# Kernel optimization log

Hardware: AMD Instinct MI355X
Metric: run time of the kernel (lower is better)

The kernel has to match this reference:

```python
import jax, jax.numpy as jnp
import numpy as np

# ---- hyperparameters (from pars / init_kwargs) ----
ALPHA = 0.9          # synaptic conductance decay (snn.Synaptic alpha)
BETA = 0.8           # membrane decay (snn.Synaptic beta)
BETA_PLUS = 0.9      # pre-synaptic trace decay
BETA_MINUS = 0.9     # post-synaptic trace decay
THRESHOLD = 1.0
W_MIN, W_MAX = 0.0, 1.0
A_PLUS, A_MINUS = 0.008, 0.0008
T, B, IN, N = 350, 128, 784, 400
SPIKE_P = 0.05       # Bernoulli firing probability of the rate-coded input


def setup_inputs() -> dict:
    key = jax.random.key(0)
    k_img, k_w = jax.random.split(key)
    # Poisson/Bernoulli rate-coded MNIST spike train [T, B, IN]
    image = (jax.random.uniform(k_img, (T, B, IN)) < SPIKE_P).astype(jnp.float32)
    # nn.Linear default init U(-1/sqrt(IN), 1/sqrt(IN)) then clamp to [w_min, w_max]
    s = 1.0 / np.sqrt(IN)
    W = jnp.clip(jax.random.uniform(k_w, (N, IN), minval=-s, maxval=s), W_MIN, W_MAX)
    return {"image": image, "W": W}


def reference(image, W):
    """Fused LIF (snntorch Synaptic, reset-by-subtraction) + STDP loop over T steps.

    Returns (W_final, mem_final, syn_final, total_spikes_per_neuron).
    """
    batch = image.shape[1]

    def step(carry, x_t):
        syn, mem, pre_tr, post_tr, W = carry
        # pre-synaptic trace: tr_t = beta_plus * tr_{t-1} + x_t
        pre_tr = BETA_PLUS * pre_tr + x_t                      # [B, IN]
        # linear projection (no bias)
        I_t = jnp.einsum('bi,ni->bn', x_t, W)                  # [B, N]
        # snntorch Synaptic: reset from pre-update mem, subtract mechanism
        reset = (mem > THRESHOLD).astype(mem.dtype)
        syn = ALPHA * syn + I_t
        mem = BETA * mem + syn - reset * THRESHOLD
        spk = (mem > THRESHOLD).astype(mem.dtype)              # [B, N]
        # post-synaptic trace
        post_tr = BETA_MINUS * post_tr + spk
        # STDP: potentiate on post spike x pre trace, depress on pre spike x post trace
        dW = (A_PLUS * jnp.einsum('bn,bi->ni', spk, pre_tr)
              - A_MINUS * jnp.einsum('bn,bi->ni', post_tr, x_t)) / batch
        W = jnp.clip(W + dW, W_MIN, W_MAX)
        return (syn, mem, pre_tr, post_tr, W), spk.sum(axis=0)

    syn0 = jnp.zeros((batch, N), image.dtype)
    mem0 = jnp.zeros((batch, N), image.dtype)
    pre0 = jnp.zeros((batch, IN), image.dtype)
    post0 = jnp.zeros((batch, N), image.dtype)

    (syn, mem, _, _, W_final), spk_counts = jax.lax.scan(
        step, (syn0, mem0, pre0, post0, W), image)
    return W_final, mem, syn, spk_counts.sum(axis=0)
```

## Files before the change

### kernel.cpp

```cpp
#include <hip/hip_runtime.h>
#include <hip/hip_bf16.h>


#define TT    350
#define BB    128
#define INF   784
#define NNEU  400
#define NS    2
#define NTHR  1024
#define LCAP  80
#define RW    13

#define ALPHA 0.9f
#define BETA  0.8f
#define BPLUS 0.9f
#define BMIN  0.9f
#define CP    (0.008f/128.0f)
#define CM    (0.0008f/128.0f)

__device__ __forceinline__ float bf2f(__hip_bfloat16 v){ return __bfloat162float(v); }

__device__ __forceinline__ void barx(){
  asm volatile("s_waitcnt lgkmcnt(0)" ::: "memory");
  __builtin_amdgcn_s_barrier();
  __builtin_amdgcn_sched_barrier(0);
}

__device__ __forceinline__ float dppred(float x){
  x += __int_as_float(__builtin_amdgcn_update_dpp(0, __float_as_int(x), 0x4E,  0xF, 0xF, true));
  x += __int_as_float(__builtin_amdgcn_update_dpp(0, __float_as_int(x), 0x124, 0xF, 0xF, true));
  x += __int_as_float(__builtin_amdgcn_update_dpp(0, __float_as_int(x), 0x128, 0xF, 0xF, true));
  return x;
}

__global__ void k_pre(const float* __restrict__ img, __hip_bfloat16* __restrict__ pre,
                      unsigned long long* __restrict__ rowm){
  int gid  = blockIdx.x*blockDim.x + threadIdx.x;
  int wid  = gid >> 6;
  int lane = gid & 63;
  if (wid >= BB*RW) return;
  int b = wid / RW, c = wid - b*RW;
  int i = c*64 + lane;
  bool has = (i < INF);
  const float* ip = img + (size_t)b*INF + i;
  __hip_bfloat16* pp = pre + (size_t)b*INF + i;
  float v = 0.f;
  for (int t=0;t<TT;t++){
    float x = has ? ip[(size_t)t*(BB*INF)] : 0.f;
    v = BPLUS*v + x;
    if (has) pp[(size_t)t*(BB*INF)] = __float2bfloat16(v);
    unsigned long long bal = __ballot(x > 0.f);
    if (lane == 0) rowm[(size_t)t*(BB*RW) + wid] = bal;
  }
}

__global__ void k_S(const __hip_bfloat16* __restrict__ pre, float* __restrict__ S){
  int idx = blockIdx.x*blockDim.x + threadIdx.x;
  if (idx >= TT*INF) return;
  int t = idx / INF, i = idx - t*INF;
  const __hip_bfloat16* p = pre + (size_t)t*(BB*INF) + i;
  float s = 0.f;
  for (int b=0;b<BB;b++) s += bf2f(p[(size_t)b*INF]);
  S[idx] = s;
}

__global__ void k_masks(const unsigned long long* __restrict__ rowm,
                        unsigned short* __restrict__ lists,
                        int* __restrict__ cnts,
                        unsigned int* __restrict__ collist){
  __shared__ unsigned long long rowbits[BB][RW];
  __shared__ unsigned short buf[16][LCAP];
  const int t = blockIdx.x;
  const int tid = threadIdx.x, lane = tid & 63, w = tid >> 6;

  for (int k = tid; k < BB*RW; k += NTHR)
    ((unsigned long long*)rowbits)[k] = rowm[(size_t)t*(BB*RW) + k];
  __syncthreads();

  for (int r8=0; r8<8; r8++){
    int r = w*8 + r8;
    int cnt = 0;
    for (int c=0;c<RW;c++){
      unsigned long long word = rowbits[r][c];
      int i = c*64 + lane;
      bool a = (word >> lane) & 1ull;
      int pos = cnt + __popcll(word & ((1ull<<lane)-1ull));
      if (a && pos < LCAP) buf[w][pos] = (unsigned short)(i<<3);
      cnt += __popcll(word);
    }
    for (int k = cnt + lane; k < LCAP; k += 64) buf[w][k] = (unsigned short)(INF<<3);
    if (lane == 0) cnts[t*BB + r] = (cnt < LCAP) ? cnt : LCAP;
    if (lane < LCAP/2)
      ((unsigned int*)(lists + (size_t)(t*BB + r)*LCAP))[lane] = ((unsigned int*)buf[w])[lane];
  }
  __syncthreads();
  if (tid < INF){
    int wsel = tid >> 6, bit = tid & 63;
    unsigned long long m0=0, m1=0;
    for (int b=0;b<64;b++) m0 |= ((rowbits[b][wsel]    >> bit) & 1ull) << b;
    for (int b=0;b<64;b++) m1 |= ((rowbits[64+b][wsel] >> bit) & 1ull) << b;
    int cnt = __popcll(m0) + __popcll(m1);
    unsigned int wd[8];
    wd[0] = (unsigned int)cnt; wd[1]=0;wd[2]=0;wd[3]=0;wd[4]=0;wd[5]=0;wd[6]=0;wd[7]=0;
    #pragma unroll
    for (int k=1;k<32;k++){
      int bb;
      if (m0){ bb = __builtin_ctzll(m0); m0 &= m0-1; }
      else if (m1){ bb = 64 + __builtin_ctzll(m1); m1 &= m1-1; }
      else bb = 128;
      wd[k>>2] |= ((unsigned int)bb) << ((k&3)*8);
    }
    uint4* dst = (uint4*)(collist + ((size_t)t*INF + tid)*8);
    uint4 lo; lo.x=wd[0]; lo.y=wd[1]; lo.z=wd[2]; lo.w=wd[3];
    uint4 hi; hi.x=wd[4]; hi.y=wd[5]; hi.z=wd[6]; hi.w=wd[7];
    dst[0]=lo; dst[1]=hi;
  }
}

__device__ __forceinline__ float potf(unsigned long long ma, unsigned long long mb,
                                      int pc, float Sv,
                                      const __hip_bfloat16* __restrict__ prt, int c){
  bool direct = (pc <= 64);
  unsigned long long m = direct ? ma : ~ma;
  unsigned long long n = direct ? mb : ~mb;
  float acc = 0.f;
  while (m){ int bb = __builtin_ctzll(m); m &= m-1; acc += bf2f(prt[(size_t)bb*INF + c]); }
  while (n){ int bb = __builtin_ctzll(n); n &= n-1; acc += bf2f(prt[(size_t)(64+bb)*INF + c]); }
  return direct ? acc : (Sv - acc);
}

#define G2(W) { float2 a_ = *(const float2*)((const char*)&Wp2[0] + ((W) & 0xffffu)); I0 += a_.x; I1 += a_.y; \
                float2 b_ = *(const float2*)((const char*)&Wp2[0] + ((W) >> 16));     I0 += b_.x; I1 += b_.y; }
#define GATHER8(V) { G2((V).x); G2((V).y); G2((V).z); G2((V).w); }

#define DEP4(W) { float2 p_; \
  p_ = postl[(W) & 0xffu];        d0 += p_.x; d1 += p_.y; \
  p_ = postl[((W)>>8) & 0xffu];   d0 += p_.x; d1 += p_.y; \
  p_ = postl[((W)>>16) & 0xffu];  d0 += p_.x; d1 += p_.y; \
  p_ = postl[(W)>>24];            d0 += p_.x; d1 += p_.y; }

__launch_bounds__(NTHR, 1)
__global__ void k_main(const float* __restrict__ Win,
                       const __hip_bfloat16* __restrict__ pre,
                       const float* __restrict__ S,
                       const unsigned short* __restrict__ lists,
                       const int* __restrict__ cnts,
                       const unsigned int* __restrict__ collist,
                       float* __restrict__ out){
  __shared__ float2 Wp2[800];
  __shared__ float2 postl[132];
  __shared__ unsigned long long smQ[2][2];
  __shared__ float cntS[2];

  const int tid  = threadIdx.x;
  const int lane = tid & 63;
  const int wv   = tid >> 6;
  const int q    = (lane >> 1) & 7;
  const int b    = (lane & 1) | (((lane >> 4) & 3) << 1) | (wv << 3);
  const int n0   = blockIdx.x * NS;

  if (tid < 800){
    float2 w;
    w.x = (tid < INF) ? Win[(size_t)n0*INF + tid] : 0.f;
    w.y = (tid < INF) ? Win[(size_t)(n0+1)*INF + tid] : 0.f;
    Wp2[tid] = w;
  }
  if (tid < 132){ postl[tid].x = 0.f; postl[tid].y = 0.f; }
  if (tid < 2) cntS[tid] = 0.f;

  const int  c0   = tid;
  const bool hasc = (c0 < INF);

  float syn0=0.f, mem0=0.f, syn1=0.f, mem1=0.f, sc0=0.f, sc1=0.f;

  uint4 lA = *(const uint4*)(lists + ((size_t)b)*LCAP + (size_t)q*8);
  int cn = cnts[b];
  uint4 cl0; cl0.x=0;cl0.y=0;cl0.z=0;cl0.w=0;
  float sv0 = 0.f;
  if (hasc){ cl0 = *(const uint4*)(collist + (size_t)c0*8); sv0 = S[c0]; }

  __syncthreads();

  for (int t=0; t<TT; t++){
    float I0 = 0.f, I1 = 0.f;
    GATHER8(lA);
    if (cn > 64 + q*8){
      uint4 lC = *(const uint4*)(lists + ((size_t)t*BB + b)*LCAP + 64 + (size_t)q*8);
      GATHER8(lC);
    }
    int tn = (t+1 < TT) ? t+1 : TT-1;
    uint4 lAn = *(const uint4*)(lists + ((size_t)tn*BB + b)*LCAP + (size_t)q*8);
    int cnn = cnts[tn*BB + b];
    uint4 cl0n = cl0; float sv0n = sv0;
    if (hasc){
      cl0n = *(const uint4*)(collist + ((size_t)tn*INF + c0)*8);
      sv0n = S[tn*INF + c0];
    }

    I0 = dppred(I0);
    I1 = dppred(I1);

    float r0 = (mem0 > 1.f) ? 1.f : 0.f;
    syn0 = ALPHA*syn0 + I0;
    mem0 = BETA*mem0 + syn0 - r0;
    float s0 = (mem0 > 1.f) ? 1.f : 0.f;
    float r1 = (mem1 > 1.f) ? 1.f : 0.f;
    syn1 = ALPHA*syn1 + I1;
    mem1 = BETA*mem1 + syn1 - r1;
    float s1 = (mem1 > 1.f) ? 1.f : 0.f;
    unsigned long long bal0 = __ballot(s0 > 0.5f);
    unsigned long long bal1 = __ballot(s1 > 0.5f);
    if (q == 0){
      sc0 += s0; sc1 += s1;
      float2 pv = postl[b];
      pv.x = BMIN*pv.x + s0;
      pv.y = BMIN*pv.y + s1;
      postl[b] = pv;
    }
    if (lane == 0){
      unsigned int by0 = (unsigned int)((bal0 & 3ull) | ((bal0>>16)&3ull)<<2 |
                                        ((bal0>>32)&3ull)<<4 | ((bal0>>48)&3ull)<<6);
      unsigned int by1 = (unsigned int)((bal1 & 3ull) | ((bal1>>16)&3ull)<<2 |
                                        ((bal1>>32)&3ull)<<4 | ((bal1>>48)&3ull)<<6);
      ((unsigned char*)smQ)[wv]      = (unsigned char)by0;
      ((unsigned char*)smQ)[16 + wv] = (unsigned char)by1;
    }
    barx();

    unsigned long long s00 = smQ[0][0], s01 = smQ[0][1];
    unsigned long long s10 = smQ[1][0], s11 = smQ[1][1];
    if (hasc){
      float d0=0.f, d1=0.f;
      unsigned int w0_ = cl0.x;
      { float2 p_;
        p_ = postl[(w0_>>8) & 0xffu];  d0 += p_.x; d1 += p_.y;
        p_ = postl[(w0_>>16) & 0xffu]; d0 += p_.x; d1 += p_.y;
        p_ = postl[w0_>>24];           d0 += p_.x; d1 += p_.y; }
      DEP4(cl0.y); DEP4(cl0.z); DEP4(cl0.w);
      int cc_ = (int)(w0_ & 0xffu);
      if (cc_ > 15){
        uint4 e2_ = *(const uint4*)(collist + ((size_t)t*INF + c0)*8 + 4);
        DEP4(e2_.x); DEP4(e2_.y); DEP4(e2_.z); DEP4(e2_.w);
      }
      int pc0 = __popcll(s00) + __popcll(s01);
      int pc1 = __popcll(s10) + __popcll(s11);
      const __hip_bfloat16* prt = pre + (size_t)t*(BB*INF);
      float pot0 = potf(s00, s01, pc0, sv0, prt, c0);
      float pot1 = potf(s10, s11, pc1, sv0, prt, c0);
      float2 wv_ = Wp2[c0];
      wv_.x = fminf(fmaxf(wv_.x + CP*pot0 - CM*d0, 0.f), 1.f);
      wv_.y = fminf(fmaxf(wv_.y + CP*pot1 - CM*d1, 0.f), 1.f);
      Wp2[c0] = wv_;
    }

    lA=lAn; cn=cnn; cl0=cl0n; sv0=sv0n;
    barx();
  }

  __syncthreads();
  if (tid < INF){
    float2 wvv = Wp2[tid];
    out[(size_t)n0*INF + tid]       = wvv.x;
    out[(size_t)(n0+1)*INF + tid]   = wvv.y;
  }
  if (q == 0){
    out[(size_t)NNEU*INF + (size_t)b*NNEU + n0]                        = mem0;
    out[(size_t)NNEU*INF + (size_t)b*NNEU + n0 + 1]                    = mem1;
    out[(size_t)NNEU*INF + (size_t)BB*NNEU + (size_t)b*NNEU + n0]      = syn0;
    out[(size_t)NNEU*INF + (size_t)BB*NNEU + (size_t)b*NNEU + n0 + 1]  = syn1;
    atomicAdd(&cntS[0], sc0);
    atomicAdd(&cntS[1], sc1);
  }
  __syncthreads();
  if (tid < 2) out[(size_t)NNEU*INF + 2*(size_t)BB*NNEU + n0 + tid] = cntS[tid];
}

extern "C" void kernel_launch(void* const* d_in, const int* in_sizes, int n_in,
                              void* d_out, int out_size, void* d_ws, size_t ws_size,
                              hipStream_t stream) {
  const float* img = (const float*)d_in[0];
  const float* W   = (const float*)d_in[1];
  float* out = (float*)d_out;

  char* ws = (char*)d_ws;
  __hip_bfloat16*     pre  = (__hip_bfloat16*)ws;
  float*              S    = (float*)(ws + 70246400);
  unsigned short*     lst  = (unsigned short*)(ws + 71344000);
  int*                cnts = (int*)(ws + 78512000);
  unsigned int*       coll = (unsigned int*)(ws + 78691200);
  unsigned long long* rowm = (unsigned long long*)(ws + 87472000);

  k_pre  <<<(BB*RW*64 + 255)/256, 256, 0, stream>>>(img, pre, rowm);
  k_S    <<<(TT*INF + 255)/256, 256, 0, stream>>>(pre, S);
  k_masks<<<TT, NTHR, 0, stream>>>(rowm, lst, cnts, coll);
  k_main <<<NNEU/NS, NTHR, 0, stream>>>(W, pre, S, lst, cnts, coll, out);
}
```

Baseline: 742.4 us.

## Build spike bitmasks from the image in parallel, then derive pre-traces from bitmasks

The serial-over-time pre-trace kernel used to read the full float image and also produce the per-row spike ballots. Now the per-timestep mask kernel reads the image in parallel across all T blocks and writes the row bitmasks itself. A new pre-trace kernel then runs the serial recurrence from the compact 64-bit masks instead of reloading the float image. This is meant to take the large image read off the serial time loop. The cost is one extra pass in which the mask kernel writes the bitmasks out to global memory.

```diff
diff --git a/kernel.cpp b/kernel.cpp
--- a/kernel.cpp
+++ b/kernel.cpp
@@ -33,50 +33,27 @@
   return x;
 }
 
-__global__ void k_pre(const float* __restrict__ img, __hip_bfloat16* __restrict__ pre,
-                      unsigned long long* __restrict__ rowm){
-  int gid  = blockIdx.x*blockDim.x + threadIdx.x;
-  int wid  = gid >> 6;
-  int lane = gid & 63;
-  if (wid >= BB*RW) return;
-  int b = wid / RW, c = wid - b*RW;
-  int i = c*64 + lane;
-  bool has = (i < INF);
-  const float* ip = img + (size_t)b*INF + i;
-  __hip_bfloat16* pp = pre + (size_t)b*INF + i;
-  float v = 0.f;
-  for (int t=0;t<TT;t++){
-    float x = has ? ip[(size_t)t*(BB*INF)] : 0.f;
-    v = BPLUS*v + x;
-    if (has) pp[(size_t)t*(BB*INF)] = __float2bfloat16(v);
-    unsigned long long bal = __ballot(x > 0.f);
-    if (lane == 0) rowm[(size_t)t*(BB*RW) + wid] = bal;
-  }
-}
-
-__global__ void k_S(const __hip_bfloat16* __restrict__ pre, float* __restrict__ S){
-  int idx = blockIdx.x*blockDim.x + threadIdx.x;
-  if (idx >= TT*INF) return;
-  int t = idx / INF, i = idx - t*INF;
-  const __hip_bfloat16* p = pre + (size_t)t*(BB*INF) + i;
-  float s = 0.f;
-  for (int b=0;b<BB;b++) s += bf2f(p[(size_t)b*INF]);
-  S[idx] = s;
-}
-
-__global__ void k_masks(const unsigned long long* __restrict__ rowm,
+__global__ void k_masks(const float* __restrict__ img,
                         unsigned short* __restrict__ lists,
                         int* __restrict__ cnts,
-                        unsigned int* __restrict__ collist){
+                        unsigned int* __restrict__ collist,
+                        unsigned long long* __restrict__ rowm){
   __shared__ unsigned long long rowbits[BB][RW];
   __shared__ unsigned short buf[16][LCAP];
   const int t = blockIdx.x;
   const int tid = threadIdx.x, lane = tid & 63, w = tid >> 6;
-
-  for (int k = tid; k < BB*RW; k += NTHR)
-    ((unsigned long long*)rowbits)[k] = rowm[(size_t)t*(BB*RW) + k];
-  __syncthreads();
-
+  const float* base = img + (size_t)t*(BB*INF);
+
+  for (int r8=0; r8<8; r8++){
+    int r = w*8 + r8;
+    const float* p = base + (size_t)r*INF;
+    for (int c=0;c<RW;c++){
+      int i = c*64 + lane;
+      bool a = (i < INF) && (p[i] > 0.f);
+      unsigned long long bal = __ballot(a);
+      if (lane == 0) rowbits[r][c] = bal;
+    }
+  }
   for (int r8=0; r8<8; r8++){
     int r = w*8 + r8;
     int cnt = 0;
@@ -94,6 +71,8 @@
       ((unsigned int*)(lists + (size_t)(t*BB + r)*LCAP))[lane] = ((unsigned int*)buf[w])[lane];
   }
   __syncthreads();
+  for (int k = tid; k < BB*RW; k += NTHR)
+    rowm[(size_t)t*(BB*RW) + k] = ((unsigned long long*)rowbits)[k];
   if (tid < INF){
     int wsel = tid >> 6, bit = tid & 63;
     unsigned long long m0=0, m1=0;
@@ -115,6 +94,36 @@
     uint4 hi; hi.x=wd[4]; hi.y=wd[5]; hi.z=wd[6]; hi.w=wd[7];
     dst[0]=lo; dst[1]=hi;
   }
+}
+
+__global__ void k_pretr(const unsigned long long* __restrict__ rowm,
+                        __hip_bfloat16* __restrict__ pre){
+  int gid  = blockIdx.x*blockDim.x + threadIdx.x;
+  int wid  = gid >> 6;
+  int lane = gid & 63;
+  if (wid >= BB*RW) return;
+  int b = wid / RW, c = wid - b*RW;
+  int i = c*64 + lane;
+  bool has = (i < INF);
+  __hip_bfloat16* pp = pre + (size_t)b*INF + i;
+  float v = 0.f;
+  #pragma unroll 2
+  for (int t=0;t<TT;t++){
+    unsigned long long word = rowm[(size_t)t*(BB*RW) + wid];
+    float x = (float)(int)((word >> lane) & 1ull);
+    v = BPLUS*v + x;
+    if (has) pp[(size_t)t*(BB*INF)] = __float2bfloat16(v);
+  }
+}
+
+__global__ void k_S(const __hip_bfloat16* __restrict__ pre, float* __restrict__ S){
+  int idx = blockIdx.x*blockDim.x + threadIdx.x;
+  if (idx >= TT*INF) return;
+  int t = idx / INF, i = idx - t*INF;
+  const __hip_bfloat16* p = pre + (size_t)t*(BB*INF) + i;
+  float s = 0.f;
+  for (int b=0;b<BB;b++) s += bf2f(p[(size_t)b*INF]);
+  S[idx] = s;
 }
 
 __device__ __forceinline__ float potf(unsigned long long ma, unsigned long long mb,
@@ -290,8 +299,8 @@
   unsigned int*       coll = (unsigned int*)(ws + 78691200);
   unsigned long long* rowm = (unsigned long long*)(ws + 87472000);
 
-  k_pre  <<<(BB*RW*64 + 255)/256, 256, 0, stream>>>(img, pre, rowm);
+  k_masks<<<TT, NTHR, 0, stream>>>(img, lst, cnts, coll, rowm);
+  k_pretr<<<(BB*RW*64 + 255)/256, 256, 0, stream>>>(rowm, pre);
   k_S    <<<(TT*INF + 255)/256, 256, 0, stream>>>(pre, S);
-  k_masks<<<TT, NTHR, 0, stream>>>(rowm, lst, cnts, coll);
   k_main <<<NNEU/NS, NTHR, 0, stream>>>(W, pre, S, lst, cnts, coll, out);
 }
```

New measurement: 786.4 us. +5.9%, slower.
